# Performance work log

Measured on AMD Instinct MI355X. Metric: run time of the kernel, lower is better.

## Reference

```python
import jax, jax.numpy as jnp
import numpy as np

B, S, ENC, DEC, ATTN = 64, 2048, 512, 512, 256

def setup_inputs() -> dict:
    key = jax.random.key(0)
    k1, k2, k3, k4, k5 = jax.random.split(key, 5)
    s = 0.05
    return {
        "enc_outputs": jax.random.normal(k1, (B, S, ENC), dtype=jnp.float32),
        "dec_state": jax.random.normal(k2, (B, DEC), dtype=jnp.float32),
        "W_enc": jax.random.normal(k3, (ENC, ATTN), dtype=jnp.float32) * s,
        "W_dec": jax.random.normal(k4, (DEC, ATTN), dtype=jnp.float32) * s,
        "v": jax.random.normal(k5, (ATTN,), dtype=jnp.float32) * s,
    }

def reference(enc_outputs, dec_state, W_enc, W_dec, v):
    # enc_proj: [B,S,A], dec_proj: [B,1,A]
    enc_proj = jnp.einsum('bse,ea->bsa', enc_outputs, W_enc)
    dec_proj = jnp.einsum('bd,da->ba', dec_state, W_dec)[:, None, :]
    scores = jnp.einsum('bsa,a->bs', jnp.tanh(enc_proj + dec_proj), v)  # [B,S]
    attn_weights = jax.nn.softmax(scores, axis=-1)
    context = jnp.einsum('bs,bse->be', attn_weights, enc_outputs)  # [B,ENC]
    return (context, attn_weights)
```

## Files before the change

kernel.cpp:

```cpp
#include <hip/hip_runtime.h>
#include <hip/hip_bf16.h>
#include <stdint.h>

#define B_    64
#define S_    2048
#define ENC_  512
#define ATTN_ 256

typedef __bf16 bf16;
typedef bf16  bf16x8 __attribute__((ext_vector_type(8)));
typedef float f32x4  __attribute__((ext_vector_type(4)));

__device__ __forceinline__ float fexp2(float x) {
#if __has_builtin(__builtin_amdgcn_exp2f)
    return __builtin_amdgcn_exp2f(x);
#else
    return exp2f(x);
#endif
}
__device__ __forceinline__ float frcp(float x) {
#if __has_builtin(__builtin_amdgcn_rcpf)
    return __builtin_amdgcn_rcpf(x);
#else
    return 1.0f / x;
#endif
}
__device__ __forceinline__ float fast_tanh(float x) {
    float e = fexp2(x * 2.8853900817779268f);
    return 1.0f - 2.0f * frcp(e + 1.0f);
}

__global__ __launch_bounds__(256) void k_setup(const float* __restrict__ W_enc,
                                               const float* __restrict__ dec_state,
                                               const float* __restrict__ W_dec,
                                               bf16* __restrict__ WT,
                                               float* __restrict__ dp) {
    int blk = blockIdx.x;
    if (blk < 512) {
        int idx = blk * 256 + threadIdx.x;
        int n = idx >> 9;
        int k = idx & 511;
        WT[idx] = (bf16)W_enc[k * ATTN_ + n];
    } else {
        int b = blk - 512;
        int a = threadIdx.x;
        const float* ds = dec_state + b * 512;
        float acc = 0.f;
#pragma unroll 8
        for (int d = 0; d < 512; ++d)
            acc += ds[d] * W_dec[d * ATTN_ + a];
        dp[b * ATTN_ + a] = acc;
    }
}

__global__ __launch_bounds__(256, 2) void k_scores(
    const float* __restrict__ enc,
    const bf16*  __restrict__ WT,
    const float* __restrict__ dp,
    const float* __restrict__ v,
    float* __restrict__ out_scores)
{
    const int tid  = threadIdx.x;
    const int wave = tid >> 6;
    const int lane = tid & 63;
    const int l15  = lane & 15;
    const int q    = lane >> 4;
    const int row0 = blockIdx.x * 128 + wave * 32;
    const int b    = row0 >> 11;

    const f32x4 zero4 = {0.f, 0.f, 0.f, 0.f};
    f32x4 acc[2][16];
#pragma unroll
    for (int mt = 0; mt < 2; ++mt)
#pragma unroll
        for (int nt = 0; nt < 16; ++nt)
            acc[mt][nt] = zero4;

    const float* ag0 = enc + (size_t)(row0 + l15) * 512 + q * 8;
    const float* ag1 = ag0 + 16 * 512;
    const bf16*  bg  = WT + (size_t)l15 * 512 + q * 8;

    float4 a0 = *(const float4*)(ag0);
    float4 a1 = *(const float4*)(ag0 + 4);
    float4 a2 = *(const float4*)(ag1);
    float4 a3 = *(const float4*)(ag1 + 4);

    for (int ks = 0; ks < 16; ++ks) {
        int ksn = (ks < 15) ? (ks + 1) : 15;
        float4 n0 = *(const float4*)(ag0 + ksn * 32);
        float4 n1 = *(const float4*)(ag0 + ksn * 32 + 4);
        float4 n2 = *(const float4*)(ag1 + ksn * 32);
        float4 n3 = *(const float4*)(ag1 + ksn * 32 + 4);

        bf16x8 af0, af1;
        af0[0]=(bf16)a0.x; af0[1]=(bf16)a0.y; af0[2]=(bf16)a0.z; af0[3]=(bf16)a0.w;
        af0[4]=(bf16)a1.x; af0[5]=(bf16)a1.y; af0[6]=(bf16)a1.z; af0[7]=(bf16)a1.w;
        af1[0]=(bf16)a2.x; af1[1]=(bf16)a2.y; af1[2]=(bf16)a2.z; af1[3]=(bf16)a2.w;
        af1[4]=(bf16)a3.x; af1[5]=(bf16)a3.y; af1[6]=(bf16)a3.z; af1[7]=(bf16)a3.w;

#pragma unroll
        for (int h = 0; h < 2; ++h) {
            bf16x8 bfr[8];
#pragma unroll
            for (int j = 0; j < 8; ++j) {
                int nt = h * 8 + j;
                bfr[j] = *(const bf16x8*)(bg + (size_t)nt * 16 * 512 + ks * 32);
            }
#pragma unroll
            for (int j = 0; j < 8; ++j) {
                int nt = h * 8 + j;
                acc[0][nt] = __builtin_amdgcn_mfma_f32_16x16x32_bf16(af0, bfr[j], acc[0][nt], 0, 0, 0);
                acc[1][nt] = __builtin_amdgcn_mfma_f32_16x16x32_bf16(af1, bfr[j], acc[1][nt], 0, 0, 0);
            }
        }
        a0 = n0; a1 = n1; a2 = n2; a3 = n3;
    }

    float dpv[16], vv[16];
#pragma unroll
    for (int nt = 0; nt < 16; ++nt) {
        int col = nt * 16 + l15;
        dpv[nt] = dp[b * 256 + col];
        vv[nt]  = v[col];
    }
#pragma unroll
    for (int mt = 0; mt < 2; ++mt) {
#pragma unroll
        for (int r = 0; r < 4; ++r) {
            float s = 0.f;
#pragma unroll
            for (int nt = 0; nt < 16; ++nt)
                s += fast_tanh(acc[mt][nt][r] + dpv[nt]) * vv[nt];
            s += __shfl_xor(s, 1, 16);
            s += __shfl_xor(s, 2, 16);
            s += __shfl_xor(s, 4, 16);
            s += __shfl_xor(s, 8, 16);
            if (l15 == 0)
                out_scores[row0 + mt * 16 + q * 4 + r] = s;
        }
    }
}

__global__ __launch_bounds__(256) void k_softmax(float* __restrict__ attn) {
    int b = blockIdx.x;
    float* s = attn + b * 2048;
    __shared__ float red[256];
    int tid = threadIdx.x;

    float x[8];
    float mx = -1e30f;
#pragma unroll
    for (int i = 0; i < 8; ++i) { x[i] = s[tid + 256 * i]; mx = fmaxf(mx, x[i]); }
    red[tid] = mx;
    __syncthreads();
    for (int off = 128; off > 0; off >>= 1) {
        if (tid < off) red[tid] = fmaxf(red[tid], red[tid + off]);
        __syncthreads();
    }
    mx = red[0];
    __syncthreads();

    float e[8];
    float lsum = 0.f;
#pragma unroll
    for (int i = 0; i < 8; ++i) { e[i] = fexp2((x[i] - mx) * 1.4426950408889634f); lsum += e[i]; }
    red[tid] = lsum;
    __syncthreads();
    for (int off = 128; off > 0; off >>= 1) {
        if (tid < off) red[tid] += red[tid + off];
        __syncthreads();
    }
    float inv = 1.0f / red[0];
#pragma unroll
    for (int i = 0; i < 8; ++i) s[tid + 256 * i] = e[i] * inv;
}

__global__ __launch_bounds__(256) void k_context(const float* __restrict__ enc,
                                                 const float* __restrict__ attn,
                                                 float* __restrict__ partial) {
    int b    = blockIdx.x >> 3;
    int slab = blockIdx.x & 7;
    int tid  = threadIdx.x;
    int eq   = tid & 127;
    int sr   = tid >> 7;
    const float* eb = enc + ((size_t)b * 2048 + slab * 256) * 512;
    const float* w  = attn + b * 2048 + slab * 256;

    f32x4 acc = {0.f, 0.f, 0.f, 0.f};
#pragma unroll 4
    for (int s = sr; s < 256; s += 2) {
        float ws = w[s];
        f32x4 ev = *(const f32x4*)(eb + (size_t)s * 512 + eq * 4);
        acc += ev * ws;
    }
    __shared__ f32x4 red[128];
    if (sr) red[eq] = acc;
    __syncthreads();
    if (!sr) {
        acc += red[eq];
        *(f32x4*)(partial + (size_t)blockIdx.x * 512 + eq * 4) = acc;
    }
}

__global__ __launch_bounds__(128) void k_ctxred(const float* __restrict__ partial,
                                                float* __restrict__ ctx) {
    int b  = blockIdx.x;
    int eq = threadIdx.x;
    f32x4 a = {0.f, 0.f, 0.f, 0.f};
#pragma unroll
    for (int slab = 0; slab < 8; ++slab)
        a += *(const f32x4*)(partial + ((size_t)b * 8 + slab) * 512 + eq * 4);
    *(f32x4*)(ctx + b * 512 + eq * 4) = a;
}

extern "C" void kernel_launch(void* const* d_in, const int* in_sizes, int n_in,
                              void* d_out, int out_size, void* d_ws, size_t ws_size,
                              hipStream_t stream) {
    const float* enc       = (const float*)d_in[0];
    const float* dec_state = (const float*)d_in[1];
    const float* W_enc     = (const float*)d_in[2];
    const float* W_dec     = (const float*)d_in[3];
    const float* v         = (const float*)d_in[4];

    float* ctx  = (float*)d_out;
    float* attn = (float*)d_out + 64 * 512;

    char*  ws      = (char*)d_ws;
    bf16*  WT      = (bf16*)ws;
    float* dp      = (float*)(ws + 256 * 1024);
    float* partial = (float*)(ws + 256 * 1024 + 64 * 1024);

    k_setup  <<<576, 256, 0, stream>>>(W_enc, dec_state, W_dec, WT, dp);
    k_scores <<<1024, 256, 0, stream>>>(enc, WT, dp, v, attn);
    k_softmax<<<64, 256, 0, stream>>>(attn);
    k_context<<<512, 256, 0, stream>>>(enc, attn, partial);
    k_ctxred <<<64, 128, 0, stream>>>(partial, ctx);
}
```

Baseline: 523.6 us.

## Stage score GEMM tiles in LDS with async B loads and 2x2 wave tiling

Rewrites the score kernel so each block stages a 128-row A tile (converted to bf16) and the full 256-column B tile per k-step in shared memory. B is loaded with global_load_lds async copies into a swizzled layout. Waves then compute a 64x128 sub-tile each instead of 32x256. Per-wave partial tanh·v sums are combined through shared memory. This removes redundant per-wave global reads of W_enc and improves reuse, at the cost of two barriers per k-step and no software prefetch of the next tile.

```diff
diff --git a/kernel.cpp b/kernel.cpp
--- a/kernel.cpp
+++ b/kernel.cpp
@@ -28,6 +28,16 @@
 __device__ __forceinline__ float fast_tanh(float x) {
     float e = fexp2(x * 2.8853900817779268f);
     return 1.0f - 2.0f * frcp(e + 1.0f);
+}
+
+__device__ __forceinline__ void async_copy16(const void* g, void* l) {
+#if __has_builtin(__builtin_amdgcn_global_load_lds)
+    __builtin_amdgcn_global_load_lds(
+        (__attribute__((address_space(1))) void*)(g),
+        (__attribute__((address_space(3))) void*)(l), 16, 0, 0);
+#else
+    *(uint4*)l = *(const uint4*)g;
+#endif
 }
 
 __global__ __launch_bounds__(256) void k_setup(const float* __restrict__ W_enc,
@@ -60,84 +70,112 @@
     const float* __restrict__ v,
     float* __restrict__ out_scores)
 {
+    __shared__ __align__(16) bf16 As[128 * 40];
+    __shared__ __align__(16) bf16 Bs[256 * 32];
+    __shared__ float partial[4][64];
+
     const int tid  = threadIdx.x;
     const int wave = tid >> 6;
     const int lane = tid & 63;
     const int l15  = lane & 15;
     const int q    = lane >> 4;
-    const int row0 = blockIdx.x * 128 + wave * 32;
-    const int b    = row0 >> 11;
-
-    const f32x4 zero4 = {0.f, 0.f, 0.f, 0.f};
-    f32x4 acc[2][16];
-#pragma unroll
-    for (int mt = 0; mt < 2; ++mt)
-#pragma unroll
-        for (int nt = 0; nt < 16; ++nt)
-            acc[mt][nt] = zero4;
-
-    const float* ag0 = enc + (size_t)(row0 + l15) * 512 + q * 8;
-    const float* ag1 = ag0 + 16 * 512;
-    const bf16*  bg  = WT + (size_t)l15 * 512 + q * 8;
-
-    float4 a0 = *(const float4*)(ag0);
-    float4 a1 = *(const float4*)(ag0 + 4);
-    float4 a2 = *(const float4*)(ag1);
-    float4 a3 = *(const float4*)(ag1 + 4);
-
-    for (int ks = 0; ks < 16; ++ks) {
-        int ksn = (ks < 15) ? (ks + 1) : 15;
-        float4 n0 = *(const float4*)(ag0 + ksn * 32);
-        float4 n1 = *(const float4*)(ag0 + ksn * 32 + 4);
-        float4 n2 = *(const float4*)(ag1 + ksn * 32);
-        float4 n3 = *(const float4*)(ag1 + ksn * 32 + 4);
-
-        bf16x8 af0, af1;
-        af0[0]=(bf16)a0.x; af0[1]=(bf16)a0.y; af0[2]=(bf16)a0.z; af0[3]=(bf16)a0.w;
-        af0[4]=(bf16)a1.x; af0[5]=(bf16)a1.y; af0[6]=(bf16)a1.z; af0[7]=(bf16)a1.w;
-        af1[0]=(bf16)a2.x; af1[1]=(bf16)a2.y; af1[2]=(bf16)a2.z; af1[3]=(bf16)a2.w;
-        af1[4]=(bf16)a3.x; af1[5]=(bf16)a3.y; af1[6]=(bf16)a3.z; af1[7]=(bf16)a3.w;
-
-#pragma unroll
-        for (int h = 0; h < 2; ++h) {
-            bf16x8 bfr[8];
-#pragma unroll
-            for (int j = 0; j < 8; ++j) {
-                int nt = h * 8 + j;
-                bfr[j] = *(const bf16x8*)(bg + (size_t)nt * 16 * 512 + ks * 32);
-            }
-#pragma unroll
-            for (int j = 0; j < 8; ++j) {
-                int nt = h * 8 + j;
-                acc[0][nt] = __builtin_amdgcn_mfma_f32_16x16x32_bf16(af0, bfr[j], acc[0][nt], 0, 0, 0);
-                acc[1][nt] = __builtin_amdgcn_mfma_f32_16x16x32_bf16(af1, bfr[j], acc[1][nt], 0, 0, 0);
-            }
-        }
-        a0 = n0; a1 = n1; a2 = n2; a3 = n3;
-    }
-
-    float dpv[16], vv[16];
-#pragma unroll
-    for (int nt = 0; nt < 16; ++nt) {
-        int col = nt * 16 + l15;
+    const int m0   = blockIdx.x * 128;
+    const int b    = blockIdx.x >> 4;
+
+    const int mrow0 = (wave >> 1) * 64;
+    const int ncol0 = (wave & 1) * 128;
+
+    float dpv[8], vv[8];
+#pragma unroll
+    for (int nt = 0; nt < 8; ++nt) {
+        int col = ncol0 + nt * 16 + l15;
         dpv[nt] = dp[b * 256 + col];
         vv[nt]  = v[col];
     }
-#pragma unroll
-    for (int mt = 0; mt < 2; ++mt) {
+
+    const f32x4 zero4 = {0.f, 0.f, 0.f, 0.f};
+    f32x4 acc[4][8];
+#pragma unroll
+    for (int mt = 0; mt < 4; ++mt)
+#pragma unroll
+        for (int nt = 0; nt < 8; ++nt)
+            acc[mt][nt] = zero4;
+
+    const int arow = tid >> 1;
+    const int akc  = tid & 1;
+    const float* ag = enc + (size_t)(m0 + arow) * 512 + akc * 16;
+    bf16* as_dst = &As[arow * 40 + akc * 16];
+
+    const int bcol4 = tid >> 2;
+    const int bslot = tid & 3;
+
+    for (int ks = 0; ks < 16; ++ks) {
+#pragma unroll
+        for (int r = 0; r < 4; ++r) {
+            int c = r * 64 + bcol4;
+            int g = bslot ^ ((c + (c >> 2)) & 3);
+            async_copy16(WT + (size_t)c * 512 + ks * 32 + g * 8,
+                         &Bs[r * 2048 + tid * 8]);
+        }
+        {
+            const float* s = ag + ks * 32;
+            float4 f0 = *(const float4*)(s);
+            float4 f1 = *(const float4*)(s + 4);
+            float4 f2 = *(const float4*)(s + 8);
+            float4 f3 = *(const float4*)(s + 12);
+            bf16x8 lo, hi;
+            lo[0]=(bf16)f0.x; lo[1]=(bf16)f0.y; lo[2]=(bf16)f0.z; lo[3]=(bf16)f0.w;
+            lo[4]=(bf16)f1.x; lo[5]=(bf16)f1.y; lo[6]=(bf16)f1.z; lo[7]=(bf16)f1.w;
+            hi[0]=(bf16)f2.x; hi[1]=(bf16)f2.y; hi[2]=(bf16)f2.z; hi[3]=(bf16)f2.w;
+            hi[4]=(bf16)f3.x; hi[5]=(bf16)f3.y; hi[6]=(bf16)f3.z; hi[7]=(bf16)f3.w;
+            *(bf16x8*)(as_dst)     = lo;
+            *(bf16x8*)(as_dst + 8) = hi;
+        }
+        __syncthreads();
+
+        bf16x8 af[4];
+#pragma unroll
+        for (int mt = 0; mt < 4; ++mt) {
+            int row = mrow0 + mt * 16 + l15;
+            af[mt] = *(const bf16x8*)(&As[row * 40 + q * 8]);
+        }
+        bf16x8 bfr[8];
+#pragma unroll
+        for (int nt = 0; nt < 8; ++nt) {
+            int col = ncol0 + nt * 16 + l15;
+            int p = q ^ ((col + (col >> 2)) & 3);
+            bfr[nt] = *(const bf16x8*)(&Bs[col * 32 + p * 8]);
+        }
+#pragma unroll
+        for (int mt = 0; mt < 4; ++mt)
+#pragma unroll
+            for (int nt = 0; nt < 8; ++nt)
+                acc[mt][nt] = __builtin_amdgcn_mfma_f32_16x16x32_bf16(af[mt], bfr[nt], acc[mt][nt], 0, 0, 0);
+        __syncthreads();
+    }
+
+#pragma unroll
+    for (int mt = 0; mt < 4; ++mt) {
 #pragma unroll
         for (int r = 0; r < 4; ++r) {
             float s = 0.f;
 #pragma unroll
-            for (int nt = 0; nt < 16; ++nt)
+            for (int nt = 0; nt < 8; ++nt)
                 s += fast_tanh(acc[mt][nt][r] + dpv[nt]) * vv[nt];
             s += __shfl_xor(s, 1, 16);
             s += __shfl_xor(s, 2, 16);
             s += __shfl_xor(s, 4, 16);
             s += __shfl_xor(s, 8, 16);
             if (l15 == 0)
-                out_scores[row0 + mt * 16 + q * 4 + r] = s;
-        }
+                partial[wave][mt * 16 + q * 4 + r] = s;
+        }
+    }
+    __syncthreads();
+    if (tid < 128) {
+        int mw   = tid >> 6;
+        int rloc = tid & 63;
+        out_scores[m0 + mw * 64 + rloc] =
+            partial[mw * 2][rloc] + partial[mw * 2 + 1][rloc];
     }
 }
 
```

After: 449.9 us. -14.1%, faster.
